# Optimization experiments

Hardware: AMD Instinct MI355X
Metric: run time of the kernel (lower is better)

Reference implementation:

```python
import jax, jax.numpy as jnp
import numpy as np

ASSET_DIM = 2048
NUM_LATENTS = 32
LATENT_DIM = 64
FLAT_DIM = NUM_LATENTS * LATENT_DIM
SCALE = LATENT_DIM ** (-0.5)


def setup_inputs() -> dict:
    key = jax.random.key(0)
    ks = jax.random.split(key, 7)
    lim = 1.0 / np.sqrt(FLAT_DIM)
    z = jax.random.normal(ks[0], (ASSET_DIM, NUM_LATENTS, LATENT_DIM), dtype=jnp.float32)
    Wq = jax.random.uniform(ks[1], (FLAT_DIM, FLAT_DIM), jnp.float32, -lim, lim)
    bq = jax.random.uniform(ks[2], (FLAT_DIM,), jnp.float32, -lim, lim)
    Wk = jax.random.uniform(ks[3], (FLAT_DIM, FLAT_DIM), jnp.float32, -lim, lim)
    bk = jax.random.uniform(ks[4], (FLAT_DIM,), jnp.float32, -lim, lim)
    Wv = jax.random.uniform(ks[5], (FLAT_DIM, FLAT_DIM), jnp.float32, -lim, lim)
    bv = jax.random.uniform(ks[6], (FLAT_DIM,), jnp.float32, -lim, lim)
    return {"z": z, "Wq": Wq, "bq": bq, "Wk": Wk, "bk": bk, "Wv": Wv, "bv": bv}


def reference(z, Wq, bq, Wk, bk, Wv, bv):
    # z: (A, L, D) -> (A, F) with F = L*D
    zf = z.reshape(ASSET_DIM, FLAT_DIM)
    q = zf @ Wq.T + bq  # (A, F)
    k = zf @ Wk.T + bk  # (A, F)
    v = zf @ Wv.T + bv  # (A, F)
    scores = (q @ k.T) * SCALE          # (A, A)
    attn = jax.nn.softmax(scores, axis=-1)
    # Original does attn[:, :, None] * v[None] then sum over axis 1;
    # that is exactly attn @ v, expressed as a fused matmul here.
    h = attn @ v                        # (A, F)
    return h.reshape(ASSET_DIM, NUM_LATENTS, LATENT_DIM)
```

## Files before the change

### kernel.cpp

```cpp
#include <hip/hip_runtime.h>
#include <hip/hip_bf16.h>


#define AD 2048
#define FD 2048
constexpr float SM_SCALE = 0.125f;

typedef __attribute__((ext_vector_type(8))) short bf16x8;
typedef __attribute__((ext_vector_type(4))) float f32x4;

__device__ __forceinline__ unsigned short f2bf(float f) {
  union { float f; unsigned u; } x; x.f = f;
  unsigned r = x.u + 0x7fffu + ((x.u >> 16) & 1u);
  return (unsigned short)(r >> 16);
}

typedef __attribute__((address_space(1))) const void GVOID;
typedef __attribute__((address_space(3))) void LVOID;

__device__ __forceinline__ void gload16(const void* g, void* l) {
  __builtin_amdgcn_global_load_lds((GVOID*)g, (LVOID*)l, 16, 0, 0);
}

struct GemmArgs {
  const void* A;
  const void* B[2];
  const float* bias[2];
  void* out[2];
  float scale;
};

template<int WROWS, int WCOLS, int MREP, int NREP, int MODE, int W2,
         int NBM, int NBN, int NZ, int SBM, int SBN>
__global__ __launch_bounds__(WROWS*WCOLS*64, W2) void gemm_d(GemmArgs args) {
  constexpr int NT = WROWS * WCOLS * 64;
  constexpr int BM = WROWS * MREP * 16;
  constexpr int BN = WCOLS * NREP * 16;
  constexpr int SA = BM * 8;
  constexpr int SB = BN * 8;
  static_assert(SA >= NT && SA % NT == 0, "A staging full-coverage");
  static_assert(SB % NT == 0, "B staging full-coverage");
  constexpr int NB   = NBM * NBN * NZ;
  constexpr int SBSZ = SBM * SBN;
  constexpr int NSBM = NBM / SBM, NSBN = NBN / SBN;
  static_assert(NB % 8 == 0 && NBM % SBM == 0 && NBN % SBN == 0, "swizzle tiling");

  __shared__ __hip_bfloat16 lA[2][BM * 64];
  __shared__ __hip_bfloat16 lB[2][BN * 64];

  const int bid    = blockIdx.x;
  const int lbid   = (bid & 7) * (NB / 8) + (bid >> 3);
  const int within = lbid % SBSZ;
  const int sb     = lbid / SBSZ;
  const int z      = sb / (NSBM * NSBN);
  const int sbr    = sb % (NSBM * NSBN);
  const int sbm    = sbr % NSBM;
  const int sbn    = sbr / NSBM;
  const int bm     = sbm * SBM + within % SBM;
  const int bn     = sbn * SBN + within / SBM;

  const __hip_bfloat16* __restrict__ A = (const __hip_bfloat16*)args.A;
  const __hip_bfloat16* __restrict__ B = (const __hip_bfloat16*)args.B[z];

  const int t    = threadIdx.x;
  const int lane = t & 63;
  const int wv   = t >> 6;
  const int wr   = wv / WCOLS;
  const int wc   = wv % WCOLS;
  const int fr   = lane & 15;
  const int s2   = lane >> 4;

  f32x4 acc[MREP][NREP] = {};

  auto scol = [](int s) { return (((s & 7) ^ ((s >> 3) & 7)) * 8); };

  auto STAGE = [&](int k0, int buf) {
    #pragma unroll
    for (int r = 0; r < SA / NT; ++r) {
      const int s = t + r * NT;
      gload16(A + (size_t)(bm * BM + (s >> 3)) * FD + k0 + scol(s), &lA[buf][s * 8]);
    }
    #pragma unroll
    for (int r = 0; r < SB / NT; ++r) {
      const int s = t + r * NT;
      gload16(B + (size_t)(bn * BN + (s >> 3)) * FD + k0 + scol(s), &lB[buf][s * 8]);
    }
  };

  auto COMPUTE = [&](int buf) {
    #pragma unroll
    for (int kk = 0; kk < 2; ++kk) {
      const int ls = s2 + 4 * kk;
      bf16x8 af[MREP], bfr[NREP];
      #pragma unroll
      for (int m = 0; m < MREP; ++m) {
        const int row = wr * (MREP * 16) + m * 16 + fr;
        af[m] = *reinterpret_cast<const bf16x8*>(
            &lA[buf][row * 64 + ((ls ^ (row & 7)) * 8)]);
      }
      #pragma unroll
      for (int n = 0; n < NREP; ++n) {
        const int row = wc * (NREP * 16) + n * 16 + fr;
        bfr[n] = *reinterpret_cast<const bf16x8*>(
            &lB[buf][row * 64 + ((ls ^ (row & 7)) * 8)]);
      }
      #pragma unroll
      for (int m = 0; m < MREP; ++m)
        #pragma unroll
        for (int n = 0; n < NREP; ++n)
          acc[m][n] = __builtin_amdgcn_mfma_f32_16x16x32_bf16(af[m], bfr[n], acc[m][n], 0, 0, 0);
    }
  };

  STAGE(0, 0);
  __syncthreads();
  int cur = 0;
  for (int k0 = 64; k0 < FD; k0 += 64) {
    STAGE(k0, cur ^ 1);
    COMPUTE(cur);
    __syncthreads();
    cur ^= 1;
  }
  COMPUTE(cur);

  const float scale = args.scale;
  const float* __restrict__ bias = args.bias[z];
  const int row0 = bm * BM + wr * (MREP * 16) + (lane >> 4) * 4;
  const int col0 = bn * BN + wc * (NREP * 16) + fr;

  if constexpr (MODE == 0) {
    float* __restrict__ out = (float*)args.out[z];
    #pragma unroll
    for (int m = 0; m < MREP; ++m)
      #pragma unroll
      for (int n = 0; n < NREP; ++n) {
        const int cg = col0 + n * 16;
        #pragma unroll
        for (int j = 0; j < 4; ++j)
          out[(size_t)(row0 + m * 16 + j) * FD + cg] = acc[m][n][j] * scale;
      }
  } else if constexpr (MODE == 1) {
    __hip_bfloat16* __restrict__ out = (__hip_bfloat16*)args.out[z];
    #pragma unroll
    for (int m = 0; m < MREP; ++m)
      #pragma unroll
      for (int n = 0; n < NREP; ++n) {
        const int cg = col0 + n * 16;
        const float badd = bias[cg];
        #pragma unroll
        for (int j = 0; j < 4; ++j) {
          unsigned short b16 = f2bf(acc[m][n][j] + badd);
          out[(size_t)(row0 + m * 16 + j) * FD + cg] = *reinterpret_cast<__hip_bfloat16*>(&b16);
        }
      }
  } else {
    __hip_bfloat16* __restrict__ out = (__hip_bfloat16*)args.out[z];
    #pragma unroll
    for (int m = 0; m < MREP; ++m)
      #pragma unroll
      for (int n = 0; n < NREP; ++n) {
        const int cg = col0 + n * 16;
        const int rg = row0 + m * 16;
        const float badd = bias[cg];
        ushort4 pk;
        pk.x = f2bf(acc[m][n][0] + badd);
        pk.y = f2bf(acc[m][n][1] + badd);
        pk.z = f2bf(acc[m][n][2] + badd);
        pk.w = f2bf(acc[m][n][3] + badd);
        *reinterpret_cast<ushort4*>(out + (size_t)cg * AD + rg) = pk;
      }
  }
}

__global__ __launch_bounds__(256) void cvt_bf16(const float* __restrict__ z,
                                                const float* __restrict__ wq,
                                                const float* __restrict__ wk,
                                                const float* __restrict__ wv,
                                                __hip_bfloat16* __restrict__ dst) {
  const size_t NITEM = (size_t)4 * 4096 * 1024 / 8;
  const size_t step = (size_t)gridDim.x * blockDim.x;
  for (size_t idx = (size_t)blockIdx.x * blockDim.x + threadIdx.x; idx < NITEM; idx += step) {
    const int ten = (int)(idx >> 19);
    const size_t off = (idx & ((1u << 19) - 1)) * 8;
    const float* src = (ten == 0) ? z : (ten == 1) ? wq : (ten == 2) ? wk : wv;
    const float4 a = *reinterpret_cast<const float4*>(src + off);
    const float4 b = *reinterpret_cast<const float4*>(src + off + 4);
    union { unsigned short us[8]; int4 v; } pk;
    pk.us[0] = f2bf(a.x); pk.us[1] = f2bf(a.y); pk.us[2] = f2bf(a.z); pk.us[3] = f2bf(a.w);
    pk.us[4] = f2bf(b.x); pk.us[5] = f2bf(b.y); pk.us[6] = f2bf(b.z); pk.us[7] = f2bf(b.w);
    *reinterpret_cast<int4*>(dst + (size_t)ten * 4096 * 1024 + off) = pk.v;
  }
}

__global__ __launch_bounds__(256) void softmax_rows(const float* __restrict__ S,
                                                    __hip_bfloat16* __restrict__ P) {
  const int row = blockIdx.x;
  const int t = threadIdx.x;
  const float* s = S + (size_t)row * AD + t * 8;
  const float4 v0 = *reinterpret_cast<const float4*>(s);
  const float4 v1 = *reinterpret_cast<const float4*>(s + 4);
  float vals[8] = {v0.x, v0.y, v0.z, v0.w, v1.x, v1.y, v1.z, v1.w};

  float m = vals[0];
  #pragma unroll
  for (int j = 1; j < 8; ++j) m = fmaxf(m, vals[j]);
  #pragma unroll
  for (int off = 32; off >= 1; off >>= 1) m = fmaxf(m, __shfl_xor(m, off));

  __shared__ float redm[4], reds[4];
  if ((t & 63) == 0) redm[t >> 6] = m;
  __syncthreads();
  m = fmaxf(fmaxf(redm[0], redm[1]), fmaxf(redm[2], redm[3]));

  float e[8];
  float sum = 0.f;
  #pragma unroll
  for (int j = 0; j < 8; ++j) { e[j] = __expf(vals[j] - m); sum += e[j]; }
  #pragma unroll
  for (int off = 32; off >= 1; off >>= 1) sum += __shfl_xor(sum, off);
  if ((t & 63) == 0) reds[t >> 6] = sum;
  __syncthreads();
  sum = reds[0] + reds[1] + reds[2] + reds[3];
  const float inv = 1.f / sum;

  union { unsigned short us[8]; int4 v; } pk;
  #pragma unroll
  for (int j = 0; j < 8; ++j) pk.us[j] = f2bf(e[j] * inv);
  *reinterpret_cast<int4*>(P + (size_t)row * AD + t * 8) = pk.v;
}

extern "C" void kernel_launch(void* const* d_in, const int* in_sizes, int n_in,
                              void* d_out, int out_size, void* d_ws, size_t ws_size,
                              hipStream_t stream) {
  const float* z  = (const float*)d_in[0];
  const float* Wq = (const float*)d_in[1];
  const float* bq = (const float*)d_in[2];
  const float* Wk = (const float*)d_in[3];
  const float* bk = (const float*)d_in[4];
  const float* Wv = (const float*)d_in[5];
  const float* bv = (const float*)d_in[6];

  char* ws = (char*)d_ws;
  const size_t MB8 = (size_t)8 * 1024 * 1024;
  __hip_bfloat16* zb  = (__hip_bfloat16*)(ws);
  __hip_bfloat16* Wqb = (__hip_bfloat16*)(ws + MB8);
  __hip_bfloat16* Wkb = (__hip_bfloat16*)(ws + 2*MB8);
  __hip_bfloat16* Wvb = (__hip_bfloat16*)(ws + 3*MB8);
  __hip_bfloat16* vT  = (__hip_bfloat16*)(ws + MB8);
  float*          S   = (float*)(ws + 2*MB8);
  __hip_bfloat16* P   = (__hip_bfloat16*)(ws);
  __hip_bfloat16* qb  = (__hip_bfloat16*)d_out;
  __hip_bfloat16* kb  = (__hip_bfloat16*)d_out + (size_t)AD * FD;

  cvt_bf16<<<dim3(2048), dim3(256), 0, stream>>>(z, Wq, Wk, Wv, (__hip_bfloat16*)ws);

  {
    GemmArgs a;
    a.A = zb;
    a.B[0] = Wqb;  a.B[1] = Wkb;
    a.bias[0] = bq; a.bias[1] = bk;
    a.out[0] = qb;  a.out[1] = kb;
    a.scale = 1.0f;
    gemm_d<2, 4, 4, 2, 1, 2, 16, 16, 2, 4, 4>
        <<<dim3(512), dim3(512), 0, stream>>>(a);
  }
  {
    GemmArgs a = {};
    a.A = zb;
    a.B[0] = Wvb;
    a.bias[0] = bv;
    a.out[0] = vT;
    a.scale = 1.0f;
    gemm_d<4, 2, 2, 2, 2, 2, 16, 32, 1, 4, 8>
        <<<dim3(512), dim3(512), 0, stream>>>(a);
  }
  {
    GemmArgs a = {};
    a.A = qb;
    a.B[0] = kb;
    a.bias[0] = nullptr;
    a.out[0] = S;
    a.scale = SM_SCALE;
    gemm_d<4, 2, 2, 2, 0, 2, 16, 32, 1, 4, 8>
        <<<dim3(512), dim3(512), 0, stream>>>(a);
  }
  softmax_rows<<<dim3(AD), dim3(256), 0, stream>>>(S, P);
  {
    GemmArgs a = {};
    a.A = P;
    a.B[0] = vT;
    a.bias[0] = nullptr;
    a.out[0] = d_out;
    a.scale = 1.0f;
    gemm_d<4, 2, 2, 2, 0, 2, 16, 32, 1, 4, 8>
        <<<dim3(512), dim3(512), 0, stream>>>(a);
  }
}
```

Measured before the change: 141.0 us.

## Triple-buffer LDS staging with fine-grained vmcnt waits in GEMM main loop

Switches the GEMM K-loop from double to triple buffering, so two tiles of global-to-LDS loads stay in flight while the current tile is computed. The full __syncthreads is replaced by explicit s_waitcnt vmcnt counts plus raw s_barrier and sched_barrier fences. This is meant to hide global memory latency better and avoid draining all outstanding loads every iteration. It costs 50% more LDS, which may reduce occupancy, and relies on the vmcnt counts matching the number of issued loads.

```diff
diff --git a/kernel.cpp b/kernel.cpp
--- a/kernel.cpp
+++ b/kernel.cpp
@@ -40,13 +40,16 @@
   constexpr int SB = BN * 8;
   static_assert(SA >= NT && SA % NT == 0, "A staging full-coverage");
   static_assert(SB % NT == 0, "B staging full-coverage");
+  constexpr int CA  = SA / NT, CB = SB / NT;
+  constexpr int LPS = CA + CB;
+  constexpr int NK  = FD / 64;
   constexpr int NB   = NBM * NBN * NZ;
   constexpr int SBSZ = SBM * SBN;
   constexpr int NSBM = NBM / SBM, NSBN = NBN / SBN;
   static_assert(NB % 8 == 0 && NBM % SBM == 0 && NBN % SBN == 0, "swizzle tiling");
 
-  __shared__ __hip_bfloat16 lA[2][BM * 64];
-  __shared__ __hip_bfloat16 lB[2][BN * 64];
+  __shared__ __hip_bfloat16 lA[3][BM * 64];
+  __shared__ __hip_bfloat16 lB[3][BN * 64];
 
   const int bid    = blockIdx.x;
   const int lbid   = (bid & 7) * (NB / 8) + (bid >> 3);
@@ -74,14 +77,15 @@
 
   auto scol = [](int s) { return (((s & 7) ^ ((s >> 3) & 7)) * 8); };
 
-  auto STAGE = [&](int k0, int buf) {
-    #pragma unroll
-    for (int r = 0; r < SA / NT; ++r) {
+  auto STAGE = [&](int kt, int buf) {
+    const int k0 = kt * 64;
+    #pragma unroll
+    for (int r = 0; r < CA; ++r) {
       const int s = t + r * NT;
       gload16(A + (size_t)(bm * BM + (s >> 3)) * FD + k0 + scol(s), &lA[buf][s * 8]);
     }
     #pragma unroll
-    for (int r = 0; r < SB / NT; ++r) {
+    for (int r = 0; r < CB; ++r) {
       const int s = t + r * NT;
       gload16(B + (size_t)(bn * BN + (s >> 3)) * FD + k0 + scol(s), &lB[buf][s * 8]);
     }
@@ -112,15 +116,28 @@
     }
   };
 
-  STAGE(0, 0);
-  __syncthreads();
+  STAGE(0, 0); STAGE(1, 1);
   int cur = 0;
-  for (int k0 = 64; k0 < FD; k0 += 64) {
-    STAGE(k0, cur ^ 1);
+  for (int i = 0; i < NK - 2; ++i) {
+    STAGE(i + 2, cur == 0 ? 2 : cur - 1);
+    asm volatile("s_waitcnt vmcnt(%0)" :: "i"(2 * LPS) : "memory");
+    __builtin_amdgcn_s_barrier();
+    __builtin_amdgcn_sched_barrier(0);
     COMPUTE(cur);
-    __syncthreads();
-    cur ^= 1;
-  }
+    asm volatile("s_waitcnt lgkmcnt(0)" ::: "memory");
+    __builtin_amdgcn_sched_barrier(0);
+    __builtin_amdgcn_s_barrier();
+    __builtin_amdgcn_sched_barrier(0);
+    cur = cur == 2 ? 0 : cur + 1;
+  }
+  asm volatile("s_waitcnt vmcnt(%0)" :: "i"(LPS) : "memory");
+  __builtin_amdgcn_s_barrier();
+  __builtin_amdgcn_sched_barrier(0);
+  COMPUTE(cur);
+  cur = cur == 2 ? 0 : cur + 1;
+  asm volatile("s_waitcnt vmcnt(0)" ::: "memory");
+  __builtin_amdgcn_s_barrier();
+  __builtin_amdgcn_sched_barrier(0);
   COMPUTE(cur);
 
   const float scale = args.scale;
```

After: 166.2 us. 1.18x slower.
